# Performance work log

Measured on AMD Instinct MI355X. Metric: run time of the kernel, lower is better.

## Reference

```python
import jax, jax.numpy as jnp
import numpy as np
import math

EMBED_DIM = 256
NUM_HEADS = 8
NUM_LEVELS = 4
NUM_POINTS = 4
HEAD_DIM = EMBED_DIM // NUM_HEADS
SPATIAL_SHAPES = np.array([[100, 100], [50, 50], [25, 25], [13, 13]], dtype=np.int64)
LEN_V = int((SPATIAL_SHAPES[:, 0] * SPATIAL_SHAPES[:, 1]).sum())  # 13294
BS, LEN_Q = 8, 1024


def _grid_sample_bilinear(img, grid):
    """img: [N, C, H, W]; grid: [N, Hg, Wg, 2] in [-1,1].
    bilinear, padding_mode='zeros', align_corners=False. Returns [N, Hg, Wg, C]."""
    N, C, H, W = img.shape
    x = (grid[..., 0] + 1.0) * (W * 0.5) - 0.5
    y = (grid[..., 1] + 1.0) * (H * 0.5) - 0.5
    x0 = jnp.floor(x)
    y0 = jnp.floor(y)
    x1 = x0 + 1.0
    y1 = y0 + 1.0
    wx1 = x - x0
    wx0 = 1.0 - wx1
    wy1 = y - y0
    wy0 = 1.0 - wy1
    b = jnp.arange(N)[:, None, None]

    def gather(yi, xi):
        valid = (yi >= 0) & (yi <= H - 1) & (xi >= 0) & (xi <= W - 1)
        yc = jnp.clip(yi, 0, H - 1).astype(jnp.int32)
        xc = jnp.clip(xi, 0, W - 1).astype(jnp.int32)
        v = img[b, :, yc, xc]  # [N, Hg, Wg, C]
        return v * valid[..., None].astype(img.dtype)

    out = (gather(y0, x0) * (wy0 * wx0)[..., None]
           + gather(y0, x1) * (wy0 * wx1)[..., None]
           + gather(y1, x0) * (wy1 * wx0)[..., None]
           + gather(y1, x1) * (wy1 * wx1)[..., None])
    return out


def _offset_bias_init():
    # Faithful to _reset_parameters: per-head directional grid init for offsets bias.
    thetas = np.arange(NUM_HEADS, dtype=np.float32) * (2.0 * math.pi / NUM_HEADS)
    g = np.stack([np.cos(thetas), np.sin(thetas)], -1)
    g = g / np.abs(g).max(-1, keepdims=True)
    g = np.tile(g.reshape(NUM_HEADS, 1, 1, 2), (1, NUM_LEVELS, NUM_POINTS, 1))
    g = g * np.arange(1, NUM_POINTS + 1, dtype=np.float32).reshape(1, 1, -1, 1)
    return jnp.asarray(g.reshape(-1))


def setup_inputs() -> dict:
    key = jax.random.key(0)
    ks = jax.random.split(key, 8)
    TP = NUM_HEADS * NUM_LEVELS * NUM_POINTS  # 128

    def xavier(k, fan_in, fan_out):
        lim = math.sqrt(6.0 / (fan_in + fan_out))
        return jax.random.uniform(k, (fan_in, fan_out), jnp.float32, -lim, lim)

    return {
        "query": jax.random.normal(ks[0], (BS, LEN_Q, EMBED_DIM), jnp.float32),
        "reference_points": jax.random.uniform(ks[1], (BS, LEN_Q, NUM_LEVELS, 2), jnp.float32),
        "value": jax.random.normal(ks[2], (BS, LEN_V, EMBED_DIM), jnp.float32),
        "value_spatial_shapes": SPATIAL_SHAPES,
        # small random weights (instead of the zero-init) so the math paths are exercised
        "so_w": 0.01 * jax.random.normal(ks[3], (EMBED_DIM, TP * 2), jnp.float32),
        "so_b": _offset_bias_init(),
        "aw_w": 0.01 * jax.random.normal(ks[4], (EMBED_DIM, TP), jnp.float32),
        "aw_b": jnp.zeros((TP,), jnp.float32),
        "vp_w": xavier(ks[5], EMBED_DIM, EMBED_DIM),
        "vp_b": jnp.zeros((EMBED_DIM,), jnp.float32),
        "op_w": xavier(ks[6], EMBED_DIM, EMBED_DIM),
        "op_b": jnp.zeros((EMBED_DIM,), jnp.float32),
    }


def reference(query, reference_points, value, value_spatial_shapes,
              so_w, so_b, aw_w, aw_b, vp_w, vp_b, op_w, op_b):
    shapes = np.asarray(value_spatial_shapes)  # static python ints
    bs, len_q, D = query.shape
    H, L, P, hd = NUM_HEADS, NUM_LEVELS, NUM_POINTS, HEAD_DIM

    v = value @ vp_w + vp_b                              # [bs, len_v, D]
    v = v.reshape(bs, -1, H, hd)                         # [bs, len_v, H, hd]

    so = (query @ so_w + so_b).reshape(bs, len_q, H, L, P, 2)
    aw = (query @ aw_w + aw_b).reshape(bs, len_q, H, L * P)
    aw = jax.nn.softmax(aw, axis=-1).reshape(bs, len_q, H, L, P)

    # reference_points last dim == 2 branch: normalize offsets by (w, h) per level
    norm = jnp.asarray(shapes[:, ::-1].copy(), dtype=query.dtype).reshape(1, 1, 1, L, 1, 2)
    loc = reference_points.reshape(bs, len_q, 1, L, 1, 2) + so / norm
    grids = 2.0 * loc - 1.0                              # [bs, len_q, H, L, P, 2]
    grids = grids.transpose(0, 2, 1, 3, 4, 5).reshape(bs * H, len_q, L, P, 2)

    samples = []
    start = 0
    for lvl in range(L):
        h, w = int(shapes[lvl, 0]), int(shapes[lvl, 1])
        vl = v[:, start:start + h * w]                   # [bs, hw, H, hd]
        start += h * w
        img = vl.transpose(0, 2, 3, 1).reshape(bs * H, hd, h, w)
        s = _grid_sample_bilinear(img, grids[:, :, lvl])  # [bs*H, len_q, P, hd]
        samples.append(s)
    samp = jnp.stack(samples, axis=2)                    # [bs*H, len_q, L, P, hd]

    w_ = aw.transpose(0, 2, 1, 3, 4).reshape(bs * H, len_q, L, P)
    out = jnp.einsum('nqlpd,nqlp->nqd', samp, w_)        # [bs*H, len_q, hd]
    out = out.reshape(bs, H, len_q, hd).transpose(0, 2, 1, 3).reshape(bs, len_q, D)
    return out @ op_w + op_b
```

## Files before the change

### kernel.cpp

```cpp
#include <hip/hip_runtime.h>
#include <hip/hip_bf16.h>
#include <math.h>

#define BSZ 8
#define LQ  1024
#define LV  13294
#define NH  8
#define HD  32
#define VM  (BSZ * LV)

typedef __attribute__((ext_vector_type(8))) short bf16x8;
typedef __attribute__((ext_vector_type(4))) float f32x4;

__device__ static inline unsigned short f2bf(float f) {
    unsigned int u = __float_as_uint(f);
    unsigned int r = (u + 0x7FFFu + ((u >> 16) & 1u)) >> 16;
    return (unsigned short)r;
}
__device__ static inline float bf2f(unsigned short s) {
    return __uint_as_float(((unsigned int)s) << 16);
}
__device__ static inline unsigned int pk2bf(float a, float b) {
    __hip_bfloat162 h = __float22bfloat162_rn(make_float2(a, b));
    return *(unsigned int*)&h;
}
__device__ static inline void async_load16(const void* g, void* l) {
    __builtin_amdgcn_global_load_lds(
        (const __attribute__((address_space(1))) unsigned int*)g,
        (__attribute__((address_space(3))) unsigned int*)l, 16, 0, 0);
}

__global__ __launch_bounds__(256) void wconv_kernel(
    const float* __restrict__ w0, const float* __restrict__ w1,
    unsigned short* __restrict__ t0, unsigned short* __restrict__ t1)
{
    const int n = blockIdx.x & 255;
    const int k = threadIdx.x;
    if (blockIdx.x < 256) t0[n * 256 + k] = f2bf(w0[k * 256 + n]);
    else                  t1[n * 256 + k] = f2bf(w1[k * 256 + n]);
}

__global__ __launch_bounds__(256, 4) void vproj_mfma_kernel(
    const float* __restrict__ A,
    const unsigned short* __restrict__ wT,
    const float* __restrict__ bias,
    unsigned short* __restrict__ v)
{
    __shared__ __align__(16) unsigned short Asb[2][64 * 32];
    __shared__ __align__(16) unsigned short Wsb[2][256 * 32];

    const int tid  = threadIdx.x;
    const int w    = tid >> 6;
    const int lane = tid & 63;
    const int mrow = lane & 15;
    const int quad = lane >> 4;
    const int m0   = blockIdx.x * 64;

    const int arow = tid >> 2;
    const int akof = (tid & 3) << 3;
    int gmA = m0 + arow; if (gmA >= VM) gmA = VM - 1;
    const float* aptr = A + (size_t)gmA * 256 + akof;

    f32x4 acc[4][4];
#pragma unroll
    for (int i = 0; i < 4; ++i)
#pragma unroll
        for (int j = 0; j < 4; ++j) acc[i][j] = (f32x4)0.f;

#define STAGE_A(c, buf) {                                                   \
        const float* ap = aptr + (c) * 32;                                  \
        const float4 f0 = *(const float4*)ap;                               \
        const float4 f1 = *(const float4*)(ap + 4);                         \
        uint4 pk;                                                           \
        pk.x = pk2bf(f0.x, f0.y); pk.y = pk2bf(f0.z, f0.w);                 \
        pk.z = pk2bf(f1.x, f1.y); pk.w = pk2bf(f1.z, f1.w);                 \
        *(uint4*)&Asb[buf][arow * 32 + akof] = pk;                          \
    }
#define STAGE_W(c, buf) {                                                   \
        const int k0 = (c) * 32;                                            \
        _Pragma("unroll")                                                   \
        for (int i = 0; i < 4; ++i) {                                       \
            const int nbase = i * 64 + w * 16;                              \
            const unsigned short* gp = wT + (size_t)(nbase + (lane >> 2)) * 256 \
                                      + k0 + ((lane & 3) << 3);             \
            async_load16(gp, &Wsb[buf][nbase * 32]);                        \
        }                                                                   \
    }

    STAGE_A(0, 0);
    STAGE_W(0, 0);
    __syncthreads();

    for (int c = 0; c < 8; ++c) {
        const int cur = c & 1;
        if (c < 7) {
            STAGE_A(c + 1, cur ^ 1);
            STAGE_W(c + 1, cur ^ 1);
        }
        bf16x8 af[4], wfr[4];
#pragma unroll
        for (int i = 0; i < 4; ++i)
            af[i] = *(const bf16x8*)&Asb[cur][(i * 16 + mrow) * 32 + (quad << 3)];
#pragma unroll
        for (int j = 0; j < 4; ++j)
            wfr[j] = *(const bf16x8*)&Wsb[cur][(w * 64 + j * 16 + mrow) * 32 + (quad << 3)];
#pragma unroll
        for (int i = 0; i < 4; ++i)
#pragma unroll
            for (int j = 0; j < 4; ++j)
                acc[i][j] = __builtin_amdgcn_mfma_f32_16x16x32_bf16(
                    wfr[j], af[i], acc[i][j], 0, 0, 0);
        __syncthreads();
    }
#undef STAGE_A
#undef STAGE_W

    float4 bj[4];
#pragma unroll
    for (int j = 0; j < 4; ++j)
        bj[j] = *(const float4*)(bias + w * 64 + j * 16 + quad * 4);

#pragma unroll
    for (int i = 0; i < 4; ++i) {
        const int gm = m0 + i * 16 + mrow;
        if (gm >= VM) continue;
        const unsigned int b   = (unsigned int)gm / (unsigned int)LV;
        const unsigned int pix = (unsigned int)gm - b * (unsigned int)LV;
#pragma unroll
        for (int j = 0; j < 4; ++j) {
            const int ch = w * 64 + j * 16 + quad * 4;
            const int h  = ch >> 5, cc = ch & 31;
            uint2 o;
            o.x = pk2bf(acc[i][j][0] + bj[j].x, acc[i][j][1] + bj[j].y);
            o.y = pk2bf(acc[i][j][2] + bj[j].z, acc[i][j][3] + bj[j].w);
            *(uint2*)(v + (((size_t)(b * NH + h)) * LV + pix) * HD + cc) = o;
        }
    }
}

__global__ __launch_bounds__(512, 2) void oproj_mfma_kernel(
    const unsigned short* __restrict__ Ah,
    const unsigned short* __restrict__ opT,
    const float* __restrict__ bias,
    float* __restrict__ out)
{
    const int tid  = threadIdx.x;
    const int w    = tid >> 6;
    const int lane = tid & 63;
    const int mrow = lane & 15;
    const int quad = lane >> 4;
    const int m0   = blockIdx.x * 32;

    bf16x8 wf[2][8];
#pragma unroll
    for (int j = 0; j < 2; ++j) {
        const int n = w * 32 + j * 16 + mrow;
#pragma unroll
        for (int kc = 0; kc < 8; ++kc)
            wf[j][kc] = *(const bf16x8*)(const void*)(opT + (size_t)n * 256 + kc * 32 + quad * 8);
    }
    float4 bj[2];
#pragma unroll
    for (int j = 0; j < 2; ++j)
        bj[j] = *(const float4*)(bias + w * 32 + j * 16 + quad * 4);

    f32x4 acc[2][2];
#pragma unroll
    for (int i = 0; i < 2; ++i)
#pragma unroll
        for (int j = 0; j < 2; ++j) acc[i][j] = (f32x4)0.f;

#pragma unroll
    for (int kc = 0; kc < 8; ++kc) {
        bf16x8 af[2];
#pragma unroll
        for (int i = 0; i < 2; ++i) {
            const int gm = m0 + i * 16 + mrow;
            af[i] = *(const bf16x8*)(const void*)(Ah + (size_t)gm * 256 + kc * 32 + quad * 8);
        }
#pragma unroll
        for (int i = 0; i < 2; ++i)
#pragma unroll
            for (int j = 0; j < 2; ++j)
                acc[i][j] = __builtin_amdgcn_mfma_f32_16x16x32_bf16(
                    wf[j][kc], af[i], acc[i][j], 0, 0, 0);
    }

#pragma unroll
    for (int i = 0; i < 2; ++i) {
        const int gm = m0 + i * 16 + mrow;
#pragma unroll
        for (int j = 0; j < 2; ++j) {
            float4 o;
            o.x = acc[i][j][0] + bj[j].x;
            o.y = acc[i][j][1] + bj[j].y;
            o.z = acc[i][j][2] + bj[j].z;
            o.w = acc[i][j][3] + bj[j].w;
            *(float4*)(out + (size_t)gm * 256 + w * 32 + j * 16 + quad * 4) = o;
        }
    }
}

__global__ __launch_bounds__(256) void qproj_kernel(
    const float* __restrict__ A,
    const float* __restrict__ so_w, const float* __restrict__ so_b,
    const float* __restrict__ aw_w, const float* __restrict__ aw_b,
    float* __restrict__ so_raw, float* __restrict__ aw_raw)
{
    __shared__ float As[16][68];
    __shared__ float Ws[16][68];

    const int tid = threadIdx.x;
    const int tx = tid & 15, ty = tid >> 4;
    const int m0 = blockIdx.y * 64;
    const int n0g = blockIdx.x * 64;

    const float* W; const float* bias; float* C; int N, n0;
    if (n0g < 256) { W = so_w; bias = so_b; C = so_raw; N = 256; n0 = n0g; }
    else           { W = aw_w; bias = aw_b; C = aw_raw; N = 128; n0 = n0g - 256; }

    const int ra = tid >> 2;
    const int ka = (tid & 3) << 2;
    const int rw = tid >> 4;
    const int cw = (tid & 15) << 2;

    float acc[4][4];
#pragma unroll
    for (int i = 0; i < 4; ++i)
#pragma unroll
        for (int j = 0; j < 4; ++j) acc[i][j] = 0.f;

    for (int k0 = 0; k0 < 256; k0 += 16) {
        const float4 av = *(const float4*)(A + (size_t)(m0 + ra) * 256 + (k0 + ka));
        As[ka + 0][ra] = av.x;
        As[ka + 1][ra] = av.y;
        As[ka + 2][ra] = av.z;
        As[ka + 3][ra] = av.w;
        *(float4*)&Ws[rw][cw] =
            *(const float4*)(W + (size_t)(k0 + rw) * N + (n0 + cw));
        __syncthreads();
#pragma unroll
        for (int k = 0; k < 16; ++k) {
            const float4 a4 = *(const float4*)&As[k][ty << 2];
            const float4 b4 = *(const float4*)&Ws[k][tx << 2];
            const float aa[4] = {a4.x, a4.y, a4.z, a4.w};
            const float bb[4] = {b4.x, b4.y, b4.z, b4.w};
#pragma unroll
            for (int i = 0; i < 4; ++i)
#pragma unroll
                for (int j = 0; j < 4; ++j)
                    acc[i][j] = fmaf(aa[i], bb[j], acc[i][j]);
        }
        __syncthreads();
    }

#pragma unroll
    for (int i = 0; i < 4; ++i) {
        const int row = m0 + (ty << 2) + i;
#pragma unroll
        for (int j = 0; j < 4; ++j) {
            const int col = n0 + (tx << 2) + j;
            C[(size_t)row * N + col] = acc[i][j] + bias[col];
        }
    }
}

__global__ __launch_bounds__(256) void sample_kernel(
    const unsigned short* __restrict__ v,
    const float* __restrict__ so_raw,
    const float* __restrict__ aw_raw,
    const float* __restrict__ refp,
    unsigned short* __restrict__ out_head)
{
    __shared__ __align__(16) float wts[512][4];
    __shared__ __align__(16) int   offs[512][4];
    extern __shared__ float lds_pad[];

    const int blk   = blockIdx.x;
    const int xcd   = blk & 7;
    const int j     = blk >> 3;
    const int bh    = xcd * 8 + (j >> 5);
    const int chunk = j & 31;
    const int h     = bh & 7;
    const int b     = bh >> 3;

    const int t = threadIdx.x;

#pragma unroll
    for (int rep = 0; rep < 2; ++rep) {
        const int s  = t + rep * 256;
        const int qq = s >> 4;
        const int pt = s & 15;
        const int l  = pt >> 2;
        const int p  = pt & 3;
        const int rq = b * LQ + chunk * 32 + qq;

        const int Wl = (l == 0) ? 100 : (l == 1) ? 50 : (l == 2) ? 25 : 13;
        const int st = (l == 0) ? 0 : (l == 1) ? 10000 : (l == 2) ? 12500 : 13125;
        const float invW = (l == 0) ? 0.01f : (l == 1) ? 0.02f : (l == 2) ? 0.04f
                                            : (1.0f / 13.0f);
        const float fw = (float)Wl;

        const float logit = aw_raw[rq * 128 + h * 16 + pt];
        float mx = logit;
#pragma unroll
        for (int d = 1; d < 16; d <<= 1) mx = fmaxf(mx, __shfl_xor(mx, d, 16));
        const float e = expf(logit - mx);
        float sm = e;
#pragma unroll
        for (int d = 1; d < 16; d <<= 1) sm += __shfl_xor(sm, d, 16);
        const float wgt = e / sm;

        const float rx = refp[((size_t)rq * 4 + l) * 2 + 0];
        const float ry = refp[((size_t)rq * 4 + l) * 2 + 1];
        const int soi  = rq * 256 + h * 32 + l * 8 + p * 2;
        const float sx = so_raw[soi];
        const float sy = so_raw[soi + 1];

        const float x = (rx + sx * invW) * fw - 0.5f;
        const float y = (ry + sy * invW) * fw - 0.5f;

        const float xf = floorf(x), yf = floorf(y);
        const int x0 = (int)xf, y0 = (int)yf;
        const float wx1 = x - xf, wx0 = 1.f - wx1;
        const float wy1 = y - yf, wy0 = 1.f - wy1;

        const float vx0 = (x0 >= 0 && x0 < Wl) ? 1.f : 0.f;
        const float vx1 = (x0 + 1 >= 0 && x0 + 1 < Wl) ? 1.f : 0.f;
        const float vy0 = (y0 >= 0 && y0 < Wl) ? 1.f : 0.f;
        const float vy1 = (y0 + 1 >= 0 && y0 + 1 < Wl) ? 1.f : 0.f;

        const int xc0 = min(max(x0, 0), Wl - 1);
        const int xc1 = min(max(x0 + 1, 0), Wl - 1);
        const int yc0 = min(max(y0, 0), Wl - 1);
        const int yc1 = min(max(y0 + 1, 0), Wl - 1);

        const int row0 = st + yc0 * Wl;
        const int row1 = st + yc1 * Wl;

        wts[s][0] = wgt * wy0 * wx0 * vy0 * vx0;
        wts[s][1] = wgt * wy0 * wx1 * vy0 * vx1;
        wts[s][2] = wgt * wy1 * wx0 * vy1 * vx0;
        wts[s][3] = wgt * wy1 * wx1 * vy1 * vx1;
        offs[s][0] = (row0 + xc0) * HD;
        offs[s][1] = (row0 + xc1) * HD;
        offs[s][2] = (row1 + xc0) * HD;
        offs[s][3] = (row1 + xc1) * HD;
    }
    __syncthreads();

    const int qq = t >> 3;
    const int ln = t & 7;
    const unsigned short* vb = v + (size_t)bh * (LV * HD) + ln * 4;

    float a0 = 0.f, a1 = 0.f, a2 = 0.f, a3 = 0.f;

#pragma unroll 4
    for (int pt = 0; pt < 16; ++pt) {
        const int s = qq * 16 + pt;
        const float4 w4 = *(const float4*)&wts[s][0];
        const int4   o4 = *(const int4*)&offs[s][0];

        const ushort4 u0 = *(const ushort4*)(vb + o4.x);
        const ushort4 u1 = *(const ushort4*)(vb + o4.y);
        const ushort4 u2 = *(const ushort4*)(vb + o4.z);
        const ushort4 u3 = *(const ushort4*)(vb + o4.w);

        a0 = fmaf(w4.x, bf2f(u0.x), a0);
        a1 = fmaf(w4.x, bf2f(u0.y), a1);
        a2 = fmaf(w4.x, bf2f(u0.z), a2);
        a3 = fmaf(w4.x, bf2f(u0.w), a3);
        a0 = fmaf(w4.y, bf2f(u1.x), a0);
        a1 = fmaf(w4.y, bf2f(u1.y), a1);
        a2 = fmaf(w4.y, bf2f(u1.z), a2);
        a3 = fmaf(w4.y, bf2f(u1.w), a3);
        a0 = fmaf(w4.z, bf2f(u2.x), a0);
        a1 = fmaf(w4.z, bf2f(u2.y), a1);
        a2 = fmaf(w4.z, bf2f(u2.z), a2);
        a3 = fmaf(w4.z, bf2f(u2.w), a3);
        a0 = fmaf(w4.w, bf2f(u3.x), a0);
        a1 = fmaf(w4.w, bf2f(u3.y), a1);
        a2 = fmaf(w4.w, bf2f(u3.z), a2);
        a3 = fmaf(w4.w, bf2f(u3.w), a3);
    }

    const int rq = b * LQ + chunk * 32 + qq;
    uint2 o;
    o.x = pk2bf(a0, a1);
    o.y = pk2bf(a2, a3);
    *(uint2*)(out_head + (size_t)rq * 256 + (h << 5) + (ln << 2)) = o;
}

extern "C" void kernel_launch(void* const* d_in, const int* in_sizes, int n_in,
                              void* d_out, int out_size, void* d_ws, size_t ws_size,
                              hipStream_t stream)
{
    const float* query = (const float*)d_in[0];
    const float* refp  = (const float*)d_in[1];
    const float* value = (const float*)d_in[2];
    const float* so_w  = (const float*)d_in[4];
    const float* so_b  = (const float*)d_in[5];
    const float* aw_w  = (const float*)d_in[6];
    const float* aw_b  = (const float*)d_in[7];
    const float* vp_w  = (const float*)d_in[8];
    const float* vp_b  = (const float*)d_in[9];
    const float* op_w  = (const float*)d_in[10];
    const float* op_b  = (const float*)d_in[11];
    float* out = (float*)d_out;

    float* ws = (float*)d_ws;
    size_t off = 0;
    unsigned short* v = (unsigned short*)(ws + off);
    off += (size_t)BSZ * NH * LV * HD / 2;
    unsigned short* wTv = (unsigned short*)(ws + off); off += 32768;
    unsigned short* wTo = (unsigned short*)(ws + off); off += 32768;
    float* so_raw = ws + off; off += (size_t)BSZ * LQ * 256;
    float* aw_raw = ws + off; off += (size_t)BSZ * LQ * 128;
    unsigned short* out_head = (unsigned short*)(ws + off);
    off += (size_t)BSZ * LQ * 256 / 2;

    wconv_kernel<<<512, 256, 0, stream>>>(vp_w, op_w, wTv, wTo);

    vproj_mfma_kernel<<<(VM + 63) / 64, 256, 0, stream>>>(value, wTv, vp_b, v);

    {
        dim3 grid(6, BSZ * LQ / 64);
        qproj_kernel<<<grid, 256, 0, stream>>>(query, so_w, so_b, aw_w, aw_b,
                                               so_raw, aw_raw);
    }
    sample_kernel<<<BSZ * NH * (LQ / 32), 256, 24576, stream>>>(
        v, so_raw, aw_raw, refp, out_head);

    oproj_mfma_kernel<<<BSZ * LQ / 32, 512, 0, stream>>>(out_head, wTo, op_b, out);
}
```

Before: 271.9 us.

## Restructure vproj staging, oproj weight loads, and sampling to wave-per-query

After: 275.5 us. Within noise of the previous version (+1.3%).

```diff
diff --git a/kernel.cpp b/kernel.cpp
--- a/kernel.cpp
+++ b/kernel.cpp
@@ -24,11 +24,6 @@
     __hip_bfloat162 h = __float22bfloat162_rn(make_float2(a, b));
     return *(unsigned int*)&h;
 }
-__device__ static inline void async_load16(const void* g, void* l) {
-    __builtin_amdgcn_global_load_lds(
-        (const __attribute__((address_space(1))) unsigned int*)g,
-        (__attribute__((address_space(3))) unsigned int*)l, 16, 0, 0);
-}
 
 __global__ __launch_bounds__(256) void wconv_kernel(
     const float* __restrict__ w0, const float* __restrict__ w1,
@@ -46,8 +41,7 @@
     const float* __restrict__ bias,
     unsigned short* __restrict__ v)
 {
-    __shared__ __align__(16) unsigned short Asb[2][64 * 32];
-    __shared__ __align__(16) unsigned short Wsb[2][256 * 32];
+    __shared__ __align__(16) unsigned short Asb[64 * 256];
 
     const int tid  = threadIdx.x;
     const int w    = tid >> 6;
@@ -56,10 +50,25 @@
     const int quad = lane >> 4;
     const int m0   = blockIdx.x * 64;
 
-    const int arow = tid >> 2;
-    const int akof = (tid & 3) << 3;
-    int gmA = m0 + arow; if (gmA >= VM) gmA = VM - 1;
-    const float* aptr = A + (size_t)gmA * 256 + akof;
+    {
+        const int row = tid >> 2;
+        const int seg = tid & 3;
+        int gm = m0 + row; if (gm >= VM) gm = VM - 1;
+        const float* ap = A + (size_t)gm * 256 + seg * 64;
+        unsigned short* lrow = &Asb[row * 256];
+#pragma unroll
+        for (int u = 0; u < 8; ++u) {
+            const float4 f0 = *(const float4*)(ap + u * 8);
+            const float4 f1 = *(const float4*)(ap + u * 8 + 4);
+            uint4 pk;
+            pk.x = pk2bf(f0.x, f0.y); pk.y = pk2bf(f0.z, f0.w);
+            pk.z = pk2bf(f1.x, f1.y); pk.w = pk2bf(f1.z, f1.w);
+            const int c  = seg * 8 + u;
+            const int cp = c ^ (row & 31);
+            *(uint4*)(lrow + cp * 8) = pk;
+        }
+    }
+    __syncthreads();
 
     f32x4 acc[4][4];
 #pragma unroll
@@ -67,53 +76,27 @@
 #pragma unroll
         for (int j = 0; j < 4; ++j) acc[i][j] = (f32x4)0.f;
 
-#define STAGE_A(c, buf) {                                                   \
-        const float* ap = aptr + (c) * 32;                                  \
-        const float4 f0 = *(const float4*)ap;                               \
-        const float4 f1 = *(const float4*)(ap + 4);                         \
-        uint4 pk;                                                           \
-        pk.x = pk2bf(f0.x, f0.y); pk.y = pk2bf(f0.z, f0.w);                 \
-        pk.z = pk2bf(f1.x, f1.y); pk.w = pk2bf(f1.z, f1.w);                 \
-        *(uint4*)&Asb[buf][arow * 32 + akof] = pk;                          \
-    }
-#define STAGE_W(c, buf) {                                                   \
-        const int k0 = (c) * 32;                                            \
-        _Pragma("unroll")                                                   \
-        for (int i = 0; i < 4; ++i) {                                       \
-            const int nbase = i * 64 + w * 16;                              \
-            const unsigned short* gp = wT + (size_t)(nbase + (lane >> 2)) * 256 \
-                                      + k0 + ((lane & 3) << 3);             \
-            async_load16(gp, &Wsb[buf][nbase * 32]);                        \
-        }                                                                   \
-    }
-
-    STAGE_A(0, 0);
-    STAGE_W(0, 0);
-    __syncthreads();
-
-    for (int c = 0; c < 8; ++c) {
-        const int cur = c & 1;
-        if (c < 7) {
-            STAGE_A(c + 1, cur ^ 1);
-            STAGE_W(c + 1, cur ^ 1);
-        }
-        bf16x8 af[4], wfr[4];
-#pragma unroll
-        for (int i = 0; i < 4; ++i)
-            af[i] = *(const bf16x8*)&Asb[cur][(i * 16 + mrow) * 32 + (quad << 3)];
-#pragma unroll
-        for (int j = 0; j < 4; ++j)
-            wfr[j] = *(const bf16x8*)&Wsb[cur][(w * 64 + j * 16 + mrow) * 32 + (quad << 3)];
+#pragma unroll
+    for (int kc = 0; kc < 8; ++kc) {
+        bf16x8 wfr[4], af[4];
+#pragma unroll
+        for (int j = 0; j < 4; ++j) {
+            const int n = w * 64 + j * 16 + mrow;
+            wfr[j] = *(const bf16x8*)(const void*)(wT + (size_t)n * 256 + kc * 32 + quad * 8);
+        }
+#pragma unroll
+        for (int i = 0; i < 4; ++i) {
+            const int mr = i * 16 + mrow;
+            const int cp = (kc * 4 + quad) ^ (mr & 31);
+            af[i] = *(const bf16x8*)(const void*)&Asb[mr * 256 + cp * 8];
+        }
 #pragma unroll
         for (int i = 0; i < 4; ++i)
 #pragma unroll
             for (int j = 0; j < 4; ++j)
                 acc[i][j] = __builtin_amdgcn_mfma_f32_16x16x32_bf16(
                     wfr[j], af[i], acc[i][j], 0, 0, 0);
-        __syncthreads();
-    }
-#undef STAGE_A
-#undef STAGE_W
+    }
 
     float4 bj[4];
 #pragma unroll
@@ -151,14 +134,6 @@
     const int quad = lane >> 4;
     const int m0   = blockIdx.x * 32;
 
-    bf16x8 wf[2][8];
-#pragma unroll
-    for (int j = 0; j < 2; ++j) {
-        const int n = w * 32 + j * 16 + mrow;
-#pragma unroll
-        for (int kc = 0; kc < 8; ++kc)
-            wf[j][kc] = *(const bf16x8*)(const void*)(opT + (size_t)n * 256 + kc * 32 + quad * 8);
-    }
     float4 bj[2];
 #pragma unroll
     for (int j = 0; j < 2; ++j)
@@ -172,7 +147,12 @@
 
 #pragma unroll
     for (int kc = 0; kc < 8; ++kc) {
-        bf16x8 af[2];
+        bf16x8 wf[2], af[2];
+#pragma unroll
+        for (int j = 0; j < 2; ++j) {
+            const int n = w * 32 + j * 16 + mrow;
+            wf[j] = *(const bf16x8*)(const void*)(opT + (size_t)n * 256 + kc * 32 + quad * 8);
+        }
 #pragma unroll
         for (int i = 0; i < 2; ++i) {
             const int gm = m0 + i * 16 + mrow;
@@ -183,7 +163,7 @@
 #pragma unroll
             for (int j = 0; j < 2; ++j)
                 acc[i][j] = __builtin_amdgcn_mfma_f32_16x16x32_bf16(
-                    wf[j][kc], af[i], acc[i][j], 0, 0, 0);
+                    wf[j], af[i], acc[i][j], 0, 0, 0);
     }
 
 #pragma unroll
@@ -272,28 +252,45 @@
     const float* __restrict__ refp,
     unsigned short* __restrict__ out_head)
 {
-    __shared__ __align__(16) float wts[512][4];
-    __shared__ __align__(16) int   offs[512][4];
-    extern __shared__ float lds_pad[];
-
-    const int blk   = blockIdx.x;
-    const int xcd   = blk & 7;
-    const int j     = blk >> 3;
-    const int bh    = xcd * 8 + (j >> 5);
-    const int chunk = j & 31;
-    const int h     = bh & 7;
-    const int b     = bh >> 3;
-
-    const int t = threadIdx.x;
-
-#pragma unroll
-    for (int rep = 0; rep < 2; ++rep) {
-        const int s  = t + rep * 256;
-        const int qq = s >> 4;
-        const int pt = s & 15;
+    const int blk = blockIdx.x;
+    const int xcd = blk & 7;
+    const int j   = blk >> 3;
+    const int bh  = xcd * 8 + (j >> 8);
+    const int qg  = j & 255;
+    const int b   = bh >> 3;
+    const int h   = bh & 7;
+
+    const int wv   = threadIdx.x >> 6;
+    const int lane = threadIdx.x & 63;
+    const int ch   = lane & 7;
+    const int pz   = lane >> 3;
+
+    const int q  = qg * 4 + wv;
+    const int rq = b * LQ + q;
+
+    const float l0 = aw_raw[rq * 128 + h * 16 + pz];
+    const float l1 = aw_raw[rq * 128 + h * 16 + 8 + pz];
+    float mx = fmaxf(l0, l1);
+    mx = fmaxf(mx, __shfl_xor(mx, 8));
+    mx = fmaxf(mx, __shfl_xor(mx, 16));
+    mx = fmaxf(mx, __shfl_xor(mx, 32));
+    const float e0 = __expf(l0 - mx), e1 = __expf(l1 - mx);
+    float sm = e0 + e1;
+    sm += __shfl_xor(sm, 8);
+    sm += __shfl_xor(sm, 16);
+    sm += __shfl_xor(sm, 32);
+    const float inv_s = 1.f / sm;
+
+    const unsigned short* vb = v + (size_t)bh * (LV * HD) + ch * 4;
+
+    float a0 = 0.f, a1 = 0.f, a2 = 0.f, a3 = 0.f;
+
+#pragma unroll
+    for (int r = 0; r < 2; ++r) {
+        const int pt = r * 8 + pz;
         const int l  = pt >> 2;
         const int p  = pt & 3;
-        const int rq = b * LQ + chunk * 32 + qq;
+        const float wgt = (r ? e1 : e0) * inv_s;
 
         const int Wl = (l == 0) ? 100 : (l == 1) ? 50 : (l == 2) ? 25 : 13;
         const int st = (l == 0) ? 0 : (l == 1) ? 10000 : (l == 2) ? 12500 : 13125;
@@ -301,24 +298,11 @@
                                             : (1.0f / 13.0f);
         const float fw = (float)Wl;
 
-        const float logit = aw_raw[rq * 128 + h * 16 + pt];
-        float mx = logit;
-#pragma unroll
-        for (int d = 1; d < 16; d <<= 1) mx = fmaxf(mx, __shfl_xor(mx, d, 16));
-        const float e = expf(logit - mx);
-        float sm = e;
-#pragma unroll
-        for (int d = 1; d < 16; d <<= 1) sm += __shfl_xor(sm, d, 16);
-        const float wgt = e / sm;
-
-        const float rx = refp[((size_t)rq * 4 + l) * 2 + 0];
-        const float ry = refp[((size_t)rq * 4 + l) * 2 + 1];
-        const int soi  = rq * 256 + h * 32 + l * 8 + p * 2;
-        const float sx = so_raw[soi];
-        const float sy = so_raw[soi + 1];
-
-        const float x = (rx + sx * invW) * fw - 0.5f;
-        const float y = (ry + sy * invW) * fw - 0.5f;
+        const float2 rxy = *(const float2*)(refp + (size_t)rq * 8 + l * 2);
+        const float2 sxy = *(const float2*)(so_raw + (size_t)rq * 256 + h * 32 + l * 8 + p * 2);
+
+        const float x = (rxy.x + sxy.x * invW) * fw - 0.5f;
+        const float y = (rxy.y + sxy.y * invW) * fw - 0.5f;
 
         const float xf = floorf(x), yf = floorf(y);
         const int x0 = (int)xf, y0 = (int)yf;
@@ -335,60 +319,50 @@
         const int yc0 = min(max(y0, 0), Wl - 1);
         const int yc1 = min(max(y0 + 1, 0), Wl - 1);
 
-        const int row0 = st + yc0 * Wl;
-        const int row1 = st + yc1 * Wl;
-
-        wts[s][0] = wgt * wy0 * wx0 * vy0 * vx0;
-        wts[s][1] = wgt * wy0 * wx1 * vy0 * vx1;
-        wts[s][2] = wgt * wy1 * wx0 * vy1 * vx0;
-        wts[s][3] = wgt * wy1 * wx1 * vy1 * vx1;
-        offs[s][0] = (row0 + xc0) * HD;
-        offs[s][1] = (row0 + xc1) * HD;
-        offs[s][2] = (row1 + xc0) * HD;
-        offs[s][3] = (row1 + xc1) * HD;
-    }
-    __syncthreads();
-
-    const int qq = t >> 3;
-    const int ln = t & 7;
-    const unsigned short* vb = v + (size_t)bh * (LV * HD) + ln * 4;
-
-    float a0 = 0.f, a1 = 0.f, a2 = 0.f, a3 = 0.f;
-
-#pragma unroll 4
-    for (int pt = 0; pt < 16; ++pt) {
-        const int s = qq * 16 + pt;
-        const float4 w4 = *(const float4*)&wts[s][0];
-        const int4   o4 = *(const int4*)&offs[s][0];
-
-        const ushort4 u0 = *(const ushort4*)(vb + o4.x);
-        const ushort4 u1 = *(const ushort4*)(vb + o4.y);
-        const ushort4 u2 = *(const ushort4*)(vb + o4.z);
-        const ushort4 u3 = *(const ushort4*)(vb + o4.w);
-
-        a0 = fmaf(w4.x, bf2f(u0.x), a0);
-        a1 = fmaf(w4.x, bf2f(u0.y), a1);
-        a2 = fmaf(w4.x, bf2f(u0.z), a2);
-        a3 = fmaf(w4.x, bf2f(u0.w), a3);
-        a0 = fmaf(w4.y, bf2f(u1.x), a0);
-        a1 = fmaf(w4.y, bf2f(u1.y), a1);
-        a2 = fmaf(w4.y, bf2f(u1.z), a2);
-        a3 = fmaf(w4.y, bf2f(u1.w), a3);
-        a0 = fmaf(w4.z, bf2f(u2.x), a0);
-        a1 = fmaf(w4.z, bf2f(u2.y), a1);
-        a2 = fmaf(w4.z, bf2f(u2.z), a2);
-        a3 = fmaf(w4.z, bf2f(u2.w), a3);
-        a0 = fmaf(w4.w, bf2f(u3.x), a0);
-        a1 = fmaf(w4.w, bf2f(u3.y), a1);
-        a2 = fmaf(w4.w, bf2f(u3.z), a2);
-        a3 = fmaf(w4.w, bf2f(u3.w), a3);
-    }
-
-    const int rq = b * LQ + chunk * 32 + qq;
-    uint2 o;
-    o.x = pk2bf(a0, a1);
-    o.y = pk2bf(a2, a3);
-    *(uint2*)(out_head + (size_t)rq * 256 + (h << 5) + (ln << 2)) = o;
+        const float w00 = wgt * wy0 * wx0 * vy0 * vx0;
+        const float w01 = wgt * wy0 * wx1 * vy0 * vx1;
+        const float w10 = wgt * wy1 * wx0 * vy1 * vx0;
+        const float w11 = wgt * wy1 * wx1 * vy1 * vx1;
+
+        const int row0 = (st + yc0 * Wl) * HD;
+        const int row1 = (st + yc1 * Wl) * HD;
+
+        const ushort4 u00 = *(const ushort4*)(vb + row0 + xc0 * HD);
+        const ushort4 u01 = *(const ushort4*)(vb + row0 + xc1 * HD);
+        const ushort4 u10 = *(const ushort4*)(vb + row1 + xc0 * HD);
+        const ushort4 u11 = *(const ushort4*)(vb + row1 + xc1 * HD);
+
+        a0 = fmaf(w00, bf2f(u00.x), a0);
+        a1 = fmaf(w00, bf2f(u00.y), a1);
+        a2 = fmaf(w00, bf2f(u00.z), a2);
+        a3 = fmaf(w00, bf2f(u00.w), a3);
+        a0 = fmaf(w01, bf2f(u01.x), a0);
+        a1 = fmaf(w01, bf2f(u01.y), a1);
+        a2 = fmaf(w01, bf2f(u01.z), a2);
+        a3 = fmaf(w01, bf2f(u01.w), a3);
+        a0 = fmaf(w10, bf2f(u10.x), a0);
+        a1 = fmaf(w10, bf2f(u10.y), a1);
+        a2 = fmaf(w10, bf2f(u10.z), a2);
+        a3 = fmaf(w10, bf2f(u10.w), a3);
+        a0 = fmaf(w11, bf2f(u11.x), a0);
+        a1 = fmaf(w11, bf2f(u11.y), a1);
+        a2 = fmaf(w11, bf2f(u11.z), a2);
+        a3 = fmaf(w11, bf2f(u11.w), a3);
+    }
+
+    a0 += __shfl_xor(a0, 8);  a1 += __shfl_xor(a1, 8);
+    a2 += __shfl_xor(a2, 8);  a3 += __shfl_xor(a3, 8);
+    a0 += __shfl_xor(a0, 16); a1 += __shfl_xor(a1, 16);
+    a2 += __shfl_xor(a2, 16); a3 += __shfl_xor(a3, 16);
+    a0 += __shfl_xor(a0, 32); a1 += __shfl_xor(a1, 32);
+    a2 += __shfl_xor(a2, 32); a3 += __shfl_xor(a3, 32);
+
+    if (pz == 0) {
+        uint2 o;
+        o.x = pk2bf(a0, a1);
+        o.y = pk2bf(a2, a3);
+        *(uint2*)(out_head + (size_t)rq * 256 + (h << 5) + (ch << 2)) = o;
+    }
 }
 
 extern "C" void kernel_launch(void* const* d_in, const int* in_sizes, int n_in,
@@ -428,7 +402,7 @@
         qproj_kernel<<<grid, 256, 0, stream>>>(query, so_w, so_b, aw_w, aw_b,
                                                so_raw, aw_raw);
     }
-    sample_kernel<<<BSZ * NH * (LQ / 32), 256, 24576, stream>>>(
+    sample_kernel<<<BSZ * NH * LQ / 4, 256, 0, stream>>>(
         v, so_raw, aw_raw, refp, out_head);
 
     oproj_mfma_kernel<<<BSZ * LQ / 32, 512, 0, stream>>>(out_head, wTo, op_b, out);
```
